# Kernel tuning notes

Measured on AMD Instinct MI355X. Metric: run time of the kernel, lower is better.

## Reference

```python
import jax, jax.numpy as jnp
import numpy as np

B, T, N, H, L, K, E, KSEL = 16, 24, 2000, 64, 2, 2, 3, 2
OUT_LEN = 24
NUM_MAT = 1 + 2 * K  # identity + K powers of each of the 2 supports


def _rw(adj):
    # random-walk matrix D^{-1} A
    d = adj.sum(axis=1)
    return adj / jnp.where(d == 0, 1.0, d)[:, None]


def _dconv(xh, A_q, A_h, W, b):
    # k-hop dual-direction diffusion convolution; xh: [b,n,f]
    feats = [xh]
    for A in (A_q, A_h):
        cur = xh
        for _ in range(K):
            cur = jnp.einsum('nm,bmf->bnf', A, cur)
            feats.append(cur)
    return jnp.concatenate(feats, axis=-1) @ W + b


def _cell(x, h, A_q, A_h, Wg, bg, Wc, bc):
    # DCRNN (diffusion-conv GRU) cell
    xh = jnp.concatenate([x, h], axis=-1)
    ru = jax.nn.sigmoid(_dconv(xh, A_q, A_h, Wg, bg))
    r, u = jnp.split(ru, 2, axis=-1)
    c = jnp.tanh(_dconv(jnp.concatenate([x, r * h], axis=-1), A_q, A_h, Wc, bc))
    return u * h + (1.0 - u) * c


def setup_inputs() -> dict:
    key = jax.random.key(0)
    ks = jax.random.split(key, 24)
    s = 0.02
    nrm = lambda k, shp: (jax.random.normal(k, shp) * s).astype(jnp.float32)
    adj = (jax.random.uniform(ks[0], (N, N)) * (jax.random.uniform(ks[1], (N, N)) < 0.05)).astype(jnp.float32)
    x_enc = jax.random.normal(ks[2], (B, T, N, 1), dtype=jnp.float32)
    x_enc = x_enc * (jax.random.uniform(ks[3], (B, T, N, 1)) < 0.7)
    x_dec = jax.random.normal(ks[4], (B, OUT_LEN, N, 1), dtype=jnp.float32)

    def cell_p(k, fin):
        k1, k2 = jax.random.split(k)
        fcat = NUM_MAT * (fin + H)
        return (nrm(k1, (fcat, 2 * H)), jnp.zeros(2 * H, jnp.float32),
                nrm(k2, (fcat, H)), jnp.zeros(H, jnp.float32))

    e0 = cell_p(ks[5], 1)
    e1 = cell_p(ks[6], H)
    d0 = cell_p(ks[7], 1)
    d1 = cell_p(ks[8], H)
    return dict(
        adj=adj, x_enc=x_enc, x_dec=x_dec,
        gate_w1=nrm(ks[9], (T, H)), gate_b1=jnp.zeros(H, jnp.float32),
        gate_w2=nrm(ks[10], (H, E)), gate_b2=jnp.zeros(E, jnp.float32),
        ew_mean=nrm(ks[11], (T, T)), eb_mean=jnp.zeros(T, jnp.float32),
        ew_wmean=nrm(ks[12], (T, T)), eb_wmean=jnp.zeros(T, jnp.float32),
        ew_diff=nrm(ks[13], (T, T)), eb_diff=jnp.zeros(T, jnp.float32),
        enc0_Wg=e0[0], enc0_bg=e0[1], enc0_Wc=e0[2], enc0_bc=e0[3],
        enc1_Wg=e1[0], enc1_bg=e1[1], enc1_Wc=e1[2], enc1_bc=e1[3],
        dec0_Wg=d0[0], dec0_bg=d0[1], dec0_Wc=d0[2], dec0_bc=d0[3],
        dec1_Wg=d1[0], dec1_bg=d1[1], dec1_Wc=d1[2], dec1_bc=d1[3],
        fc_w=nrm(ks[14], (H, 1)), fc_b=jnp.zeros(1, jnp.float32),
        epoch=10,
    )


def reference(adj, x_enc, x_dec, gate_w1, gate_b1, gate_w2, gate_b2,
              ew_mean, eb_mean, ew_wmean, eb_wmean, ew_diff, eb_diff,
              enc0_Wg, enc0_bg, enc0_Wc, enc0_bc, enc1_Wg, enc1_bg, enc1_Wc, enc1_bc,
              dec0_Wg, dec0_bg, dec0_Wc, dec0_bc, dec1_Wg, dec1_bg, dec1_Wc, dec1_bc,
              fc_w, fc_b, epoch):
    A_q = _rw(adj)
    A_h = _rw(adj.T)

    # ---- DataPreparation: MoE-gated graph imputation ----
    x = jnp.transpose(x_enc[..., 0], (0, 2, 1))  # [b, n, t]
    g = jax.nn.relu(x @ gate_w1 + gate_b1)
    logits = g @ gate_w2 + gate_b2               # [b, n, E]
    top, idx = jax.lax.top_k(logits, KSEL)
    w = jax.nn.softmax(top, axis=-1)
    gate = (w[..., None] * jax.nn.one_hot(idx, E, dtype=x.dtype)).sum(axis=-2)  # [b,n,E]

    adj_ns = adj * (1.0 - jnp.eye(N, dtype=adj.dtype))
    deg_bin = (adj_ns > 0).astype(x.dtype)
    A_mean = deg_bin / jnp.maximum(deg_bin.sum(axis=1, keepdims=True), 1.0)
    rs = adj_ns.sum(axis=1, keepdims=True)
    A_wmean = adj_ns / jnp.where(rs == 0, 1.0, rs)
    A_diff = _rw(adj_ns)

    outs = [jnp.einsum('nm,bmt->bnt', A_agg, x) @ W + b
            for A_agg, W, b in ((A_mean, ew_mean, eb_mean),
                                (A_wmean, ew_wmean, eb_wmean),
                                (A_diff, ew_diff, eb_diff))]
    combined = (gate[..., None] * jnp.stack(outs, axis=2)).sum(axis=2)  # [b,n,t]
    x = jnp.where(x == 0, combined, x)
    x_imp = jnp.transpose(x, (0, 2, 1))[..., None]  # [b,t,n,1]

    # ---- Encoder: scan over time, 2 DCRNN layers ----
    enc_params = ((enc0_Wg, enc0_bg, enc0_Wc, enc0_bc),
                  (enc1_Wg, enc1_bg, enc1_Wc, enc1_bc))

    def enc_step(h, xt):
        inp = xt
        hs = []
        for l in range(L):
            nh = _cell(inp, h[l], A_q, A_h, *enc_params[l])
            inp = nh
            hs.append(nh)
        return jnp.stack(hs), None

    h0 = jnp.zeros((L, B, N, H), x_imp.dtype)
    hT, _ = jax.lax.scan(enc_step, h0, jnp.transpose(x_imp, (1, 0, 2, 3)))

    dec_params = ((dec0_Wg, dec0_bg, dec0_Wc, dec0_bc),
                  (dec1_Wg, dec1_bg, dec1_Wc, dec1_bc))

    def dec_step(carry, _):
        inp, h = carry
        hs = []
        for l in range(L):
            nh = _cell(inp, h[l], A_q, A_h, *dec_params[l])
            inp = nh
            hs.append(nh)
        out = nh @ fc_w + fc_b  # [b,n,1]
        return (out, jnp.stack(hs)), out

    _, outs_t = jax.lax.scan(dec_step, (x_imp[:, -1], hT), None, length=OUT_LEN)
    return jnp.transpose(outs_t, (1, 0, 2, 3))  # [b, out_len, n, 1]
```

## Files before the change

kernel.cpp:

```cpp
#include <hip/hip_runtime.h>

#define NROW 2000
#define NB   16
#define NT   24
#define NH   64
#define NM   (NROW*NB)
#define HOPLDS (NROW*80)
#define ENT_CAP 262144

typedef _Float16 h16;
typedef __attribute__((ext_vector_type(2))) _Float16 h16x2;
typedef __attribute__((ext_vector_type(8))) _Float16 h16x8;
typedef __attribute__((ext_vector_type(4))) float    f32x4;

__device__ __forceinline__ h16x2 bc_h2(unsigned int u){ union{unsigned int u; h16x2 h;} c; c.u=u; return c.h; }

__global__ __launch_bounds__(256) void k_count(const float* adj, int* cnt_q, int* cnt_h, int* cnt_ns,
    float* rsum_q, float* rsum_h, float* rsum_ns, int* deg_ns){
  int wid = (blockIdx.x*256 + threadIdx.x)>>6;
  int lane = threadIdx.x & 63;
  int kind = wid / NROW, n = wid - kind*NROW;
  int cnt = 0; float sum = 0.f;
  for (int c = lane; c < NROW; c += 64){
    float v = (kind==1) ? adj[(size_t)c*NROW + n] : adj[(size_t)n*NROW + c];
    if (kind==2 && c==n) v = 0.f;
    cnt += (v != 0.f); sum += v;
  }
  for (int off=32; off; off>>=1){ cnt += __shfl_down(cnt,off); sum += __shfl_down(sum,off); }
  if (lane==0){
    int pc = (cnt+7)&~7;
    if (kind==0){ cnt_q[n]=pc; rsum_q[n]=sum; }
    else if (kind==1){ cnt_h[n]=pc; rsum_h[n]=sum; }
    else { cnt_ns[n]=pc; rsum_ns[n]=sum; deg_ns[n]=cnt; }
  }
}

__global__ __launch_bounds__(1024) void k_scan(const int* cq, const int* ch, const int* cn,
    int* rq, int* rh, int* rn){
  __shared__ int s0[2048], s1[2048], s2[2048];
  int t = threadIdx.x;
  for (int a=0;a<2;a++){ int i=t+a*1024; s0[i]= i<NROW?cq[i]:0; s1[i]= i<NROW?ch[i]:0; s2[i]= i<NROW?cn[i]:0; }
  __syncthreads();
  for (int off=1; off<2048; off<<=1){
    int v0[2],v1[2],v2[2];
    for (int a=0;a<2;a++){ int i=t+a*1024; v0[a]= i>=off? s0[i-off]:0; v1[a]= i>=off? s1[i-off]:0; v2[a]= i>=off? s2[i-off]:0; }
    __syncthreads();
    for (int a=0;a<2;a++){ int i=t+a*1024; s0[i]+=v0[a]; s1[i]+=v1[a]; s2[i]+=v2[a]; }
    __syncthreads();
  }
  for (int a=0;a<2;a++){ int i=t+a*1024; if (i<=NROW){ rq[i]= i? s0[i-1]:0; rh[i]= i? s1[i-1]:0; rn[i]= i? s2[i-1]:0; } }
}

__device__ __forceinline__ uint2 mk_ent(int c, float a){
  h16 h = (h16)a;
  unsigned short us = __builtin_bit_cast(unsigned short, h);
  return make_uint2((unsigned int)(c*80), (unsigned int)us * 0x10001u);
}

__global__ __launch_bounds__(256) void k_fill(const float* adj, const int* rptr_q, const int* rptr_h, const int* rptr_ns,
    const float* rsum_q, const float* rsum_h, const float* rsum_ns, const int* deg_ns,
    uint2* ent_q, uint2* ent_h, uint2* ent_m, uint2* ent_w){
  int wid = (blockIdx.x*256 + threadIdx.x)>>6;
  int lane = threadIdx.x & 63;
  int kind = wid / NROW, n = wid - kind*NROW;
  const int* rp = (kind==0)?rptr_q:(kind==1)?rptr_h:rptr_ns;
  int p = rp[n], pend = rp[n+1];
  float inv, invm = 0.f;
  if (kind==0){ float d = rsum_q[n]; inv = d!=0.f?1.f/d:0.f; }
  else if (kind==1){ float d = rsum_h[n]; inv = d!=0.f?1.f/d:0.f; }
  else { float d = rsum_ns[n]; inv = d!=0.f?1.f/d:0.f; int dg = deg_ns[n]; invm = 1.f/(float)(dg>1?dg:1); }
  int base = 0;
  unsigned long long below = (1ull<<lane)-1ull;
  for (int c0=0; c0<NROW; c0+=64){
    int c = c0+lane; float v = 0.f;
    if (c < NROW){ v = (kind==1)? adj[(size_t)c*NROW+n] : adj[(size_t)n*NROW+c]; if (kind==2 && c==n) v = 0.f; }
    unsigned long long m = __ballot(v != 0.f);
    if (v != 0.f){
      int pos = p + base + __popcll(m & below);
      if (kind==2){ ent_w[pos] = mk_ent(c, v*inv); ent_m[pos] = mk_ent(c, invm); }
      else if (kind==0) ent_q[pos] = mk_ent(c, v*inv);
      else              ent_h[pos] = mk_ent(c, v*inv);
    }
    base += __popcll(m);
  }
  for (int i = p+base+lane; i < pend; i += 64){
    uint2 z = make_uint2(0u,0u);
    if (kind==2){ ent_w[i]=z; ent_m[i]=z; } else if (kind==0) ent_q[i]=z; else ent_h[i]=z;
  }
}

struct HopJob { const h16* X; const int* rptr; const uint2* ent; h16* out; };

__device__ __forceinline__ void proc2(const char* xs, int cl, uint4 p, h16x2 ha[4]){
  union{f32x4 v; h16x2 h[4];} ca, cb;
  ca.v = *(const f32x4*)(xs + p.x + cl);
  cb.v = *(const f32x4*)(xs + p.z + cl);
  h16x2 va = bc_h2(p.y), vb = bc_h2(p.w);
  ha[0] = ca.h[0]*va + ha[0];
  ha[1] = ca.h[1]*va + ha[1];
  ha[2] = ca.h[2]*va + ha[2];
  ha[3] = ca.h[3]*va + ha[3];
  ha[0] = cb.h[0]*vb + ha[0];
  ha[1] = cb.h[1]*vb + ha[1];
  ha[2] = cb.h[2]*vb + ha[2];
  ha[3] = cb.h[3]*vb + ha[3];
}

__global__ __launch_bounds__(1024) void k_hop(HopJob j0, HopJob j1, HopJob j2, HopJob j3,
                                              int coltiles, int rsplit, int rows_per, int C){
  extern __shared__ char xs[];
  int per = coltiles*rsplit;
  int bid = blockIdx.x;
  int jb = bid/per, rem = bid - jb*per;
  int ct = rem/rsplit, rs = rem - ct*rsplit;
  HopJob j = (jb==0)?j0:(jb==1)?j1:(jb==2)?j2:j3;
  int c0 = ct*32;
  int tid = threadIdx.x;
  {
    int r0 = tid>>2, so = tid&3;
    const char* src = (const char*)j.X + (size_t)2*(c0 + so*8);
    char* dst = xs + so*16;
    for (int r = r0; r < NROW; r += 256)
      *(f32x4*)(dst + r*80) = *(const f32x4*)(src + (size_t)2*r*C);
  }
  __syncthreads();
  int lane = tid&63, wv = tid>>6;
  int g = lane>>2;
  int cl = (lane&3)*16;
  int rbase = rs*rows_per;
  int rend = rbase + rows_per; if (rend > NROW) rend = NROW;
  int units = (rows_per+15)>>4;
  for (int u = wv; u < units; u += 16){
    int n = rbase + u*16 + g;
    if (n < rend){
      int p0 = j.rptr[n], cnt = j.rptr[n+1]-p0;
      const uint4* ep4 = (const uint4*)(j.ent + p0);
      float f[8] = {0.f,0.f,0.f,0.f,0.f,0.f,0.f,0.f};
      if (cnt > 0){
        uint4 e0 = ep4[0], e1 = ep4[1], e2 = ep4[2], e3 = ep4[3];
        for (int i=0; i<cnt; i+=8){
          uint4 n0,n1,n2,n3;
          if (i+8 < cnt){
            int b = (i>>1)+4;
            n0 = ep4[b]; n1 = ep4[b+1]; n2 = ep4[b+2]; n3 = ep4[b+3];
          }
          h16x2 ha[4] = {{(_Float16)0.f,(_Float16)0.f},{(_Float16)0.f,(_Float16)0.f},
                         {(_Float16)0.f,(_Float16)0.f},{(_Float16)0.f,(_Float16)0.f}};
          proc2(xs, cl, e0, ha);
          proc2(xs, cl, e1, ha);
          proc2(xs, cl, e2, ha);
          proc2(xs, cl, e3, ha);
          f[0] += (float)ha[0][0]; f[1] += (float)ha[0][1];
          f[2] += (float)ha[1][0]; f[3] += (float)ha[1][1];
          f[4] += (float)ha[2][0]; f[5] += (float)ha[2][1];
          f[6] += (float)ha[3][0]; f[7] += (float)ha[3][1];
          e0=n0; e1=n1; e2=n2; e3=n3;
        }
      }
      alignas(16) h16 ov[8];
      #pragma unroll
      for (int k2=0;k2<8;k2++) ov[k2] = (h16)f[k2];
      *(uint4*)((char*)j.out + (size_t)2*((size_t)n*C + c0) + cl) = *(const uint4*)ov;
    }
  }
}

__global__ void k_evinit(const float* rq, const float* rh, float* eq, float* eh){
  int n = blockIdx.x*256+threadIdx.x; if (n>=NROW) return;
  eq[n] = rq[n]!=0.f?1.f:0.f; eh[n] = rh[n]!=0.f?1.f:0.f;
}

__global__ __launch_bounds__(256) void k_matvec(const int* rptr, const uint2* ent, const float* vin, float* vout){
  int wid = (blockIdx.x*256+threadIdx.x)>>6; int lane = threadIdx.x&63;
  if (wid >= NROW) return;
  int p0 = rptr[wid], p1 = rptr[wid+1];
  float s = 0.f;
  for (int i=p0+lane; i<p1; i+=64){
    uint2 e = ent[i];
    int idx = (int)(e.x/80u);
    h16 hv = __builtin_bit_cast(h16, (unsigned short)(e.y & 0xffffu));
    s += (float)hv * vin[idx];
  }
  for (int off=32; off; off>>=1) s += __shfl_down(s,off);
  if (lane==0) vout[wid] = s;
}

__global__ void k_bias2(const float* W, const float* fcb, const float* e1, const float* e2,
                        const float* e3, const float* e4, float* dst, int O){
  int idx = blockIdx.x*256+threadIdx.x; if (idx >= NROW*O) return;
  int n = idx/O, o = idx - n*O;
  float v = W[o] + e1[n]*W[(size_t)65*O+o] + e2[n]*W[(size_t)130*O+o]
                 + e3[n]*W[(size_t)195*O+o] + e4[n]*W[(size_t)260*O+o];
  dst[idx] = fcb[0]*v;
}

__global__ void k_wpack(const float* W, const float* fcw, h16* dst, int O, int nch, int mode){
  int idx = blockIdx.x*256+threadIdx.x; if (idx >= nch*O*32) return;
  int k = idx&31; int o = (idx>>5)%O; int ch = idx/(O*32);
  float v = 0.f;
  if (mode==0){
    if (ch < 10){ int m = ch>>1, j = (ch&1)*32 + k; v = W[(size_t)(m*65+1+j)*O + o]; }
    else if (k < 5) v = W[(size_t)(k*65)*O + o];
  } else if (mode==1){
    int m = ch>>2, j = (ch&3)*32 + k; v = W[(size_t)(m*128+j)*O + o];
  } else {
    if (ch < 10){ int m = ch>>1, j = (ch&1)*32 + k; v = fcw[j]*W[(size_t)(m*65)*O + o]; }
    else { int c2 = ch-10; int m = c2>>1, j = (c2&1)*32 + k; v = W[(size_t)(m*65+1+j)*O + o]; }
  }
  dst[(size_t)(ch*O + o)*32 + k] = (h16)v;
}

__global__ __launch_bounds__(256) void k_impute_gate(const float* x_enc, const float* gw1, const float* gb1,
    const float* gw2, const float* gb2, float* gate3, h16* xT){
  int tid = blockIdx.x*256+threadIdx.x; if (tid >= NM) return;
  int b = tid / NROW, n = tid - b*NROW;
  float x24[NT];
  #pragma unroll
  for (int t=0;t<NT;t++) x24[t] = x_enc[((size_t)b*NT+t)*NROW + n];
  float acc[NH];
  #pragma unroll
  for (int h=0;h<NH;h++) acc[h] = gb1[h];
  for (int t=0;t<NT;t++){
    float xv = x24[t];
    #pragma unroll
    for (int h=0;h<NH;h++) acc[h] = fmaf(xv, gw1[t*NH+h], acc[h]);
  }
  #pragma unroll
  for (int h=0;h<NH;h++) acc[h] = fmaxf(acc[h], 0.f);
  float lg[3];
  #pragma unroll
  for (int e=0;e<3;e++){
    float s = gb2[e];
    #pragma unroll
    for (int h=0;h<NH;h++) s = fmaf(acc[h], gw2[h*3+e], s);
    lg[e] = s;
  }
  int i0 = 0; if (lg[1] > lg[0]) i0 = 1; if (lg[2] > lg[i0]) i0 = 2;
  int i1 = (i0==0)?1:0;
  for (int e=0;e<3;e++) if (e!=i0 && e!=i1 && lg[e] > lg[i1]) i1 = e;
  float w1 = expf(lg[i1]-lg[i0]);
  float s = 1.f + w1;
  float g[3] = {0.f,0.f,0.f};
  g[i0] = 1.f/s; g[i1] = w1/s;
  gate3[tid*3+0]=g[0]; gate3[tid*3+1]=g[1]; gate3[tid*3+2]=g[2];
  h16* xp = xT + ((size_t)n*NB + b)*NT;
  #pragma unroll
  for (int t=0;t<NT;t++) xp[t] = (h16)x24[t];
}

__global__ __launch_bounds__(256) void k_impute_combine(const float* x_enc, const h16* Zm, const h16* Zw,
    const float* gate3, const float* ewm, const float* ebm, const float* eww, const float* ebw,
    const float* ewd, const float* ebd, h16* ximp){
  int tid = blockIdx.x*256+threadIdx.x; if (tid >= NM) return;
  int b = tid / NROW, n = tid - b*NROW;
  float x24[NT], zm[NT], zw[NT];
  const h16* zp1 = Zm + ((size_t)n*NB+b)*NT;
  const h16* zp2 = Zw + ((size_t)n*NB+b)*NT;
  #pragma unroll
  for (int t=0;t<NT;t++){ x24[t] = x_enc[((size_t)b*NT+t)*NROW + n]; zm[t]=(float)zp1[t]; zw[t]=(float)zp2[t]; }
  float g0=gate3[tid*3], g1=gate3[tid*3+1], g2=gate3[tid*3+2];
  h16* op = ximp + ((size_t)n*NB+b)*NT;
  for (int t=0;t<NT;t++){
    float am=ebm[t], aw=ebw[t], ad=ebd[t];
    #pragma unroll
    for (int ss=0;ss<NT;ss++){ am = fmaf(zm[ss], ewm[ss*NT+t], am); aw = fmaf(zw[ss], eww[ss*NT+t], aw); ad = fmaf(zw[ss], ewd[ss*NT+t], ad); }
    float comb = g0*am + g1*aw + g2*ad;
    op[t] = (h16)((x24[t]==0.f)? comb : x24[t]);
  }
}

__global__ void k_xpack8(const h16* ximp, const h16* xq1, const h16* xq2, const h16* xh1, const h16* xh2, h16* xp){
  int idx = blockIdx.x*256+threadIdx.x; if (idx >= NT*NM) return;
  int t = idx/NM, r = idx - t*NM;
  size_t s = (size_t)r*NT + t;
  alignas(16) h16 v[8] = { ximp[s], xq1[s], xq2[s], xh1[s], xh2[s], (h16)0.f,(h16)0.f,(h16)0.f };
  *(uint4*)(xp + ((size_t)t*NM + r)*8) = *(const uint4*)v;
}

struct GArgs {
  const h16* src[20];
  int rstrideB[20];
  int coffB[20];
  const h16* wpack;
  const float* bias;
  const h16* hbuf;
  h16* rhbuf;
  float* ubuf;
  h16* hout;
  const float* bias2;
  const float* fcw;
  const float* fcb;
  float* dout;
  int tstep;
  int nchunks;
  int xchunk;
};

template<int O, int GATE, int BIAS2, int FCOUT>
__global__ __launch_bounds__(256) void k_g(GArgs a){
  __shared__ h16 As[128*40];
  __shared__ h16 Bs[O*40];
  const int tid = threadIdx.x;
  const int lane = tid&63, wv = tid>>6;
  const int l15 = lane&15, l4 = lane>>4;
  const int mbase = blockIdx.x*128;
  f32x4 acc[2][O/16];
  #pragma unroll
  for (int rf=0;rf<2;rf++)
    #pragma unroll
    for (int cf=0;cf<O/16;cf++) acc[rf][cf] = (f32x4){0.f,0.f,0.f,0.f};

  f32x4 ra[2], rb[2];
  const f32x4 vz = (f32x4){0.f,0.f,0.f,0.f};
  auto loadA = [&](int ch){
    const char* sp = (const char*)a.src[ch] + a.coffB[ch] + (size_t)mbase*a.rstrideB[ch];
    if (ch == a.xchunk){
      int r = tid>>1;
      ra[1] = vz;
      ra[0] = (tid&1) ? vz : *(const f32x4*)(sp + (size_t)r*16);
    } else {
      int rs = a.rstrideB[ch];
      #pragma unroll
      for (int ps=0; ps<2; ps++){
        int flat = ps*256+tid; int r = flat>>2, q = flat&3;
        ra[ps] = *(const f32x4*)(sp + (size_t)r*rs + q*16);
      }
    }
    const char* wp = (const char*)a.wpack + (size_t)ch*O*64;
    #pragma unroll
    for (int ps=0; ps<O/64; ps++){
      int flat = ps*256+tid;
      rb[ps] = *(const f32x4*)(wp + (size_t)flat*16);
    }
  };
  auto writeA = [&](int ch){
    if (ch == a.xchunk){
      int r = tid>>1; int half = (tid&1)*32;
      *(f32x4*)((char*)As + r*80 + half)      = ra[0];
      *(f32x4*)((char*)As + r*80 + half + 16) = ra[1];
    } else {
      #pragma unroll
      for (int ps=0; ps<2; ps++){
        int flat = ps*256+tid; int r = flat>>2, q = flat&3;
        *(f32x4*)((char*)As + r*80 + q*16) = ra[ps];
      }
    }
    #pragma unroll
    for (int ps=0; ps<O/64; ps++){
      int flat = ps*256+tid; int r = flat>>2, q = flat&3;
      *(f32x4*)((char*)Bs + r*80 + q*16) = rb[ps];
    }
  };

  loadA(0);
  for (int ch=0; ch<a.nchunks; ch++){
    writeA(ch);
    __syncthreads();
    if (ch+1 < a.nchunks) loadA(ch+1);
    h16x8 a0 = *(const h16x8*)((const char*)As + (wv*32 + l15)*80 + l4*16);
    h16x8 a1 = *(const h16x8*)((const char*)As + (wv*32 + 16 + l15)*80 + l4*16);
    #pragma unroll
    for (int cf=0; cf<O/16; cf++){
      h16x8 bfr = *(const h16x8*)((const char*)Bs + (cf*16 + l15)*80 + l4*16);
      acc[0][cf] = __builtin_amdgcn_mfma_f32_16x16x32_f16(a0, bfr, acc[0][cf], 0,0,0);
      acc[1][cf] = __builtin_amdgcn_mfma_f32_16x16x32_f16(a1, bfr, acc[1][cf], 0,0,0);
    }
    __syncthreads();
  }
  float fcp[8] = {0.f,0.f,0.f,0.f,0.f,0.f,0.f,0.f};
  #pragma unroll
  for (int rf=0; rf<2; rf++){
    #pragma unroll
    for (int cf=0; cf<O/16; cf++){
      #pragma unroll
      for (int i=0;i<4;i++){
        int row = mbase + wv*32 + rf*16 + l4*4 + i;
        int col = cf*16 + l15;
        float v = acc[rf][cf][i] + a.bias[col];
        if (BIAS2) v += a.bias2[(size_t)(row>>4)*O + col];
        if (GATE){
          float sg = 1.f/(1.f+expf(-v));
          if (cf*16 < NH){
            float hv = (float)a.hbuf[(size_t)row*NH + col];
            a.rhbuf[(size_t)row*NH + col] = (h16)(sg*hv);
          } else {
            a.ubuf[(size_t)row*NH + (col-NH)] = sg;
          }
        } else {
          float cc = tanhf(v);
          float u  = a.ubuf[(size_t)row*NH + col];
          float hv = (float)a.hbuf[(size_t)row*NH + col];
          float hn = u*hv + (1.f-u)*cc;
          a.hout[(size_t)row*NH + col] = (h16)hn;
          if (FCOUT) fcp[rf*4+i] += hn * a.fcw[col];
        }
      }
    }
  }
  if (FCOUT){
    #pragma unroll
    for (int k=0;k<8;k++){
      float s = fcp[k];
      s += __shfl_xor(s,1); s += __shfl_xor(s,2); s += __shfl_xor(s,4); s += __shfl_xor(s,8);
      if (l15==0){
        int rf = k>>2, i = k&3;
        int row = mbase + wv*32 + rf*16 + l4*4 + i;
        int n = row>>4, b = row&15;
        a.dout[(size_t)b*(NT*NROW) + (size_t)a.tstep*NROW + n] = s + a.fcb[0];
      }
    }
  }
}

extern "C" void kernel_launch(void* const* d_in, const int* in_sizes, int n_in,
                              void* d_out, int out_size, void* d_ws, size_t ws_size,
                              hipStream_t stream)
{
  const float* adj   = (const float*)d_in[0];
  const float* x_enc = (const float*)d_in[1];
  const float* gw1   = (const float*)d_in[3];
  const float* gb1   = (const float*)d_in[4];
  const float* gw2   = (const float*)d_in[5];
  const float* gb2   = (const float*)d_in[6];
  const float* ewm   = (const float*)d_in[7];
  const float* ebm   = (const float*)d_in[8];
  const float* eww   = (const float*)d_in[9];
  const float* ebw   = (const float*)d_in[10];
  const float* ewd   = (const float*)d_in[11];
  const float* ebd   = (const float*)d_in[12];
  const float* Wg[4] = {(const float*)d_in[13],(const float*)d_in[17],(const float*)d_in[21],(const float*)d_in[25]};
  const float* bg[4] = {(const float*)d_in[14],(const float*)d_in[18],(const float*)d_in[22],(const float*)d_in[26]};
  const float* Wc[4] = {(const float*)d_in[15],(const float*)d_in[19],(const float*)d_in[23],(const float*)d_in[27]};
  const float* bc[4] = {(const float*)d_in[16],(const float*)d_in[20],(const float*)d_in[24],(const float*)d_in[28]};
  const float* fcw   = (const float*)d_in[29];
  const float* fcb   = (const float*)d_in[30];
  float* outp = (float*)d_out;
  (void)in_sizes; (void)n_in; (void)out_size; (void)ws_size;

  char* base = (char*)d_ws;
  size_t off = 0;
  auto alloc = [&](size_t sz)->char*{ char* p = base + off; off += (sz + 255) & ~(size_t)255; return p; };

  uint2* ent_q = (uint2*)alloc(ENT_CAP*8);
  uint2* ent_h = (uint2*)alloc(ENT_CAP*8);
  uint2* ent_m = (uint2*)alloc(ENT_CAP*8);
  uint2* ent_w = (uint2*)alloc(ENT_CAP*8);
  int* rptr_q = (int*)alloc(2001*4);
  int* rptr_h = (int*)alloc(2001*4);
  int* rptr_n = (int*)alloc(2001*4);
  int* cnt_q = (int*)alloc(NROW*4);
  int* cnt_h = (int*)alloc(NROW*4);
  int* cnt_n = (int*)alloc(NROW*4);
  float* rsum_q = (float*)alloc(NROW*4);
  float* rsum_h = (float*)alloc(NROW*4);
  float* rsum_n = (float*)alloc(NROW*4);
  int* deg_n = (int*)alloc(NROW*4);
  float* evq1 = (float*)alloc(NROW*4);
  float* evq2 = (float*)alloc(NROW*4);
  float* evh1 = (float*)alloc(NROW*4);
  float* evh2 = (float*)alloc(NROW*4);
  float* gate3 = (float*)alloc((size_t)NM*3*4);
  h16* xpack = (h16*)alloc((size_t)NT*NM*8*2);
  h16* wp_e0g = (h16*)alloc(11*128*64); h16* wp_e0c = (h16*)alloc(11*64*64);
  h16* wp_e1g = (h16*)alloc(20*128*64); h16* wp_e1c = (h16*)alloc(20*64*64);
  h16* wp_d0gE= (h16*)alloc(11*128*64); h16* wp_d0cE= (h16*)alloc(11*64*64);
  h16* wp_d0gW= (h16*)alloc(20*128*64); h16* wp_d0cW= (h16*)alloc(20*64*64);
  h16* wp_d1g = (h16*)alloc(20*128*64); h16* wp_d1c = (h16*)alloc(20*64*64);
  float* bias2g = (float*)alloc((size_t)NROW*128*4);
  float* bias2c = (float*)alloc((size_t)NROW*64*4);
  const size_t SEG = (size_t)NM*NH*2;
  h16* h0 = (h16*)alloc(SEG);
  h16* h1 = (h16*)alloc(SEG);
  float* ub = (float*)alloc((size_t)NM*NH*4);
  h16* rh = (h16*)alloc(SEG);
  h16* zb = (h16*)alloc(SEG);
  h16* H0Q1=(h16*)alloc(SEG); h16* H0Q2=(h16*)alloc(SEG); h16* H0H1=(h16*)alloc(SEG); h16* H0H2=(h16*)alloc(SEG);
  h16* H1Q1=(h16*)alloc(SEG); h16* H1Q2=(h16*)alloc(SEG); h16* H1H1=(h16*)alloc(SEG); h16* H1H2=(h16*)alloc(SEG);
  h16* RHQ1=(h16*)alloc(SEG); h16* RHQ2=(h16*)alloc(SEG); h16* RHH1=(h16*)alloc(SEG); h16* RHH2=(h16*)alloc(SEG);
  h16* xT   = RHQ1;  h16* Zm = RHQ2;  h16* Zw = RHH1;  h16* ximp = RHH2;
  h16* xq1  = H1Q1;  h16* xq2 = H1Q2; h16* xh1 = H1H1; h16* xh2 = H1H2;

  hipFuncSetAttribute(reinterpret_cast<const void*>(k_hop),
                      hipFuncAttributeMaxDynamicSharedMemorySize, HOPLDS);

  hipMemsetAsync(zb, 0, SEG, stream);
  hipMemsetAsync(h0, 0, SEG, stream);
  hipMemsetAsync(h1, 0, SEG, stream);

  k_count<<<1500,256,0,stream>>>(adj, cnt_q, cnt_h, cnt_n, rsum_q, rsum_h, rsum_n, deg_n);
  k_scan<<<1,1024,0,stream>>>(cnt_q, cnt_h, cnt_n, rptr_q, rptr_h, rptr_n);
  k_fill<<<1500,256,0,stream>>>(adj, rptr_q, rptr_h, rptr_n, rsum_q, rsum_h, rsum_n, deg_n,
                                ent_q, ent_h, ent_m, ent_w);
  k_evinit<<<8,256,0,stream>>>(rsum_q, rsum_h, evq1, evh1);
  k_matvec<<<500,256,0,stream>>>(rptr_q, ent_q, evq1, evq2);
  k_matvec<<<500,256,0,stream>>>(rptr_h, ent_h, evh1, evh2);
  k_bias2<<<1000,256,0,stream>>>(Wg[2], fcb, evq1, evq2, evh1, evh2, bias2g, 128);
  k_bias2<<<500,256,0,stream>>>(Wc[2], fcb, evq1, evq2, evh1, evh2, bias2c, 64);
  auto wpk = [&](const float* W, h16* dst, int O, int nch, int mode){
    k_wpack<<<(nch*O*32+255)/256,256,0,stream>>>(W, fcw, dst, O, nch, mode);
  };
  wpk(Wg[0], wp_e0g, 128, 11, 0); wpk(Wc[0], wp_e0c, 64, 11, 0);
  wpk(Wg[1], wp_e1g, 128, 20, 1); wpk(Wc[1], wp_e1c, 64, 20, 1);
  wpk(Wg[2], wp_d0gE,128, 11, 0); wpk(Wc[2], wp_d0cE,64, 11, 0);
  wpk(Wg[2], wp_d0gW,128, 20, 2); wpk(Wc[2], wp_d0cW,64, 20, 2);
  wpk(Wg[3], wp_d1g, 128, 20, 1); wpk(Wc[3], wp_d1c, 64, 20, 1);

  k_impute_gate<<<125,256,0,stream>>>(x_enc, gw1, gb1, gw2, gb2, gate3, xT);

  auto hop = [&](HopJob a, HopJob b, HopJob c, HopJob d, int nj, int C, int rsplit){
    int ct = C/32;
    k_hop<<<nj*ct*rsplit, 1024, HOPLDS, stream>>>(a,b,c,d, ct, rsplit, NROW/rsplit, C);
  };
  HopJob JA{xT, rptr_n, ent_m, Zm}, JB{xT, rptr_n, ent_w, Zw};
  hop(JA, JB, JA, JB, 2, NB*NT, 10);
  k_impute_combine<<<125,256,0,stream>>>(x_enc, Zm, Zw, gate3, ewm, ebm, eww, ebw, ewd, ebd, ximp);
  HopJob X1{ximp, rptr_q, ent_q, xq1}, X2{ximp, rptr_h, ent_h, xh1};
  hop(X1, X2, X1, X2, 2, NB*NT, 10);
  HopJob X3{xq1, rptr_q, ent_q, xq2}, X4{xh1, rptr_h, ent_h, xh2};
  hop(X3, X4, X3, X4, 2, NB*NT, 10);
  k_xpack8<<<(NT*NM+255)/256,256,0,stream>>>(ximp, xq1, xq2, xh1, xh2, xpack);

  h16* HSEG0[5] = {h0, H0Q1, H0Q2, H0H1, H0H2};
  h16* HSEG1[5] = {h1, H1Q1, H1Q2, H1H1, H1H2};
  h16* RSEG[5]  = {rh, RHQ1, RHQ2, RHH1, RHH2};
  h16* ZSEG[5]  = {zb, zb, zb, zb, zb};

  auto shapeA = [&](GArgs& A, h16* const* seg, const h16* xpk){
    for (int m=0;m<5;m++) for (int s=0;s<2;s++){ int ch=2*m+s; A.src[ch]=seg[m]; A.rstrideB[ch]=NH*2; A.coffB[ch]=s*64; }
    A.src[10]=xpk; A.rstrideB[10]=16; A.coffB[10]=0; A.nchunks=11; A.xchunk=10;
  };
  auto shapeB = [&](GArgs& A, h16* const* sa, h16* const* sb){
    for (int m=0;m<5;m++) for (int s=0;s<4;s++){ int ch=4*m+s;
      A.src[ch] = (s<2)? sa[m] : sb[m]; A.rstrideB[ch]=NH*2; A.coffB[ch]=(s&1)*64; }
    A.nchunks=20; A.xchunk=-1;
  };
  auto shapeC = [&](GArgs& A, h16* const* segH, h16* const* segX){
    for (int m=0;m<5;m++) for (int s=0;s<2;s++){
      int ch=2*m+s; A.src[ch]=segX[m]; A.rstrideB[ch]=NH*2; A.coffB[ch]=s*64;
      int c2=10+2*m+s; A.src[c2]=segH[m]; A.rstrideB[c2]=NH*2; A.coffB[c2]=s*64; }
    A.nchunks=20; A.xchunk=-1;
  };
  auto common = [&](GArgs& A, const h16* wp, const float* bias, const h16* hb, const float* b2, int t){
    A.wpack=wp; A.bias=bias; A.hbuf=hb; A.rhbuf=rh; A.ubuf=ub; A.hout=(h16*)hb;
    A.bias2=b2; A.fcw=fcw; A.fcb=fcb; A.dout=outp; A.tstep=t;
  };

  for (int phase=0; phase<2; phase++){
    int ig = phase? 2 : 0;
    const h16* wpg0E = phase? wp_d0gE : wp_e0g;
    const h16* wpc0E = phase? wp_d0cE : wp_e0c;
    const h16* wpg1  = phase? wp_d1g  : wp_e1g;
    const h16* wpc1  = phase? wp_d1c  : wp_e1c;
    for (int t=0;t<NT;t++){
      bool wprime = (phase==1 && t>0);
      if (wprime){
        HopJob a{h1, rptr_q, ent_q, H1Q1}, b{h1, rptr_h, ent_h, H1H1};
        hop(a,b,a,b, 2, NB*NH, 4);
        HopJob c{H1Q1, rptr_q, ent_q, H1Q2}, d{H1H1, rptr_h, ent_h, H1H2};
        hop(c,d,c,d, 2, NB*NH, 4);
      }
      {
        GArgs A{};
        if (wprime) shapeC(A, HSEG0, HSEG1);
        else shapeA(A, (phase==0 && t==0)? ZSEG : HSEG0, xpack + (size_t)((phase==0)? t : 23)*NM*8);
        common(A, wprime? wp_d0gW : wpg0E, bg[ig], h0, bias2g, t);
        if (wprime) k_g<128,1,1,0><<<250,256,0,stream>>>(A);
        else        k_g<128,1,0,0><<<250,256,0,stream>>>(A);
      }
      if (wprime){
        HopJob a{rh, rptr_q, ent_q, RHQ1}, b{rh, rptr_h, ent_h, RHH1};
        hop(a,b,a,b, 2, NB*NH, 4);
        HopJob c{RHQ1, rptr_q, ent_q, RHQ2}, d{RHH1, rptr_h, ent_h, RHH2};
        hop(c,d,c,d, 2, NB*NH, 4);
      } else {
        HopJob a{rh, rptr_q, ent_q, RHQ1}, b{rh, rptr_h, ent_h, RHH1};
        HopJob c{h1, rptr_q, ent_q, H1Q1}, d{h1, rptr_h, ent_h, H1H1};
        hop(a,b,c,d, 4, NB*NH, 2);
        HopJob a2{RHQ1, rptr_q, ent_q, RHQ2}, b2{RHH1, rptr_h, ent_h, RHH2};
        HopJob c2{H1Q1, rptr_q, ent_q, H1Q2}, d2{H1H1, rptr_h, ent_h, H1H2};
        hop(a2,b2,c2,d2, 4, NB*NH, 2);
      }
      {
        GArgs A{};
        if (wprime) shapeC(A, RSEG, HSEG1);
        else shapeA(A, RSEG, xpack + (size_t)((phase==0)? t : 23)*NM*8);
        common(A, wprime? wp_d0cW : wpc0E, bc[ig], h0, bias2c, t);
        if (wprime) k_g<64,0,1,0><<<250,256,0,stream>>>(A);
        else        k_g<64,0,0,0><<<250,256,0,stream>>>(A);
      }
      {
        HopJob a{h0, rptr_q, ent_q, H0Q1}, b{h0, rptr_h, ent_h, H0H1};
        hop(a,b,a,b, 2, NB*NH, 4);
        HopJob c{H0Q1, rptr_q, ent_q, H0Q2}, d{H0H1, rptr_h, ent_h, H0H2};
        hop(c,d,c,d, 2, NB*NH, 4);
      }
      {
        GArgs A{};
        shapeB(A, HSEG0, HSEG1);
        common(A, wpg1, bg[ig+1], h1, nullptr, t);
        k_g<128,1,0,0><<<250,256,0,stream>>>(A);
      }
      {
        HopJob a{rh, rptr_q, ent_q, RHQ1}, b{rh, rptr_h, ent_h, RHH1};
        hop(a,b,a,b, 2, NB*NH, 4);
        HopJob c{RHQ1, rptr_q, ent_q, RHQ2}, d{RHH1, rptr_h, ent_h, RHH2};
        hop(c,d,c,d, 2, NB*NH, 4);
      }
      {
        GArgs A{};
        shapeB(A, HSEG0, RSEG);
        common(A, wpc1, bc[ig+1], h1, nullptr, t);
        if (phase) k_g<64,0,0,1><<<250,256,0,stream>>>(A);
        else       k_g<64,0,0,0><<<250,256,0,stream>>>(A);
      }
    }
  }
}
```

Baseline: 16.19 ms.

## Halve GEMM row tile, unroll hop gather loop, unpad hop LDS rows

Three changes. The GEMM kernel's M tile drops from 128 to 64 rows per block, with one MFMA fragment per wave and 500 blocks instead of 250, to spread work over more CUs and lower register pressure. The sparse hop kernel now processes 16 entries per iteration with 8-deep prefetch and a tail of up to 8 entries. Its LDS row stride drops from 80 to 64 bytes, so index decoding becomes a shift instead of a divide, at the risk of LDS bank conflicts. Deeper prefetch raises register use in the hop kernel, and the smaller GEMM tile gives less reuse of weight tiles per block.

Result: faster. 13.50 ms (-16.6%).

```diff
diff --git a/kernel.cpp b/kernel.cpp
--- a/kernel.cpp
+++ b/kernel.cpp
@@ -5,7 +5,7 @@
 #define NT   24
 #define NH   64
 #define NM   (NROW*NB)
-#define HOPLDS (NROW*80)
+#define HOPLDS (NROW*64)
 #define ENT_CAP 262144
 
 typedef _Float16 h16;
@@ -54,7 +54,7 @@
 __device__ __forceinline__ uint2 mk_ent(int c, float a){
   h16 h = (h16)a;
   unsigned short us = __builtin_bit_cast(unsigned short, h);
-  return make_uint2((unsigned int)(c*80), (unsigned int)us * 0x10001u);
+  return make_uint2((unsigned int)(c*64), (unsigned int)us * 0x10001u);
 }
 
 __global__ __launch_bounds__(256) void k_fill(const float* adj, const int* rptr_q, const int* rptr_h, const int* rptr_ns,
@@ -121,7 +121,7 @@
     const char* src = (const char*)j.X + (size_t)2*(c0 + so*8);
     char* dst = xs + so*16;
     for (int r = r0; r < NROW; r += 256)
-      *(f32x4*)(dst + r*80) = *(const f32x4*)(src + (size_t)2*r*C);
+      *(f32x4*)(dst + r*64) = *(const f32x4*)(src + (size_t)2*r*C);
   }
   __syncthreads();
   int lane = tid&63, wv = tid>>6;
@@ -137,24 +137,37 @@
       const uint4* ep4 = (const uint4*)(j.ent + p0);
       float f[8] = {0.f,0.f,0.f,0.f,0.f,0.f,0.f,0.f};
       if (cnt > 0){
-        uint4 e0 = ep4[0], e1 = ep4[1], e2 = ep4[2], e3 = ep4[3];
-        for (int i=0; i<cnt; i+=8){
-          uint4 n0,n1,n2,n3;
-          if (i+8 < cnt){
-            int b = (i>>1)+4;
-            n0 = ep4[b]; n1 = ep4[b+1]; n2 = ep4[b+2]; n3 = ep4[b+3];
-          }
+        uint4 cur[8];
+        #pragma unroll
+        for (int u2=0;u2<8;u2++) cur[u2] = ep4[u2];
+        int i = 0;
+        for (; i+16 <= cnt; i += 16){
+          uint4 nx[8];
+          int b = (i>>1)+8;
+          #pragma unroll
+          for (int u2=0;u2<8;u2++) nx[u2] = ep4[b+u2];
           h16x2 ha[4] = {{(_Float16)0.f,(_Float16)0.f},{(_Float16)0.f,(_Float16)0.f},
                          {(_Float16)0.f,(_Float16)0.f},{(_Float16)0.f,(_Float16)0.f}};
-          proc2(xs, cl, e0, ha);
-          proc2(xs, cl, e1, ha);
-          proc2(xs, cl, e2, ha);
-          proc2(xs, cl, e3, ha);
+          #pragma unroll
+          for (int u2=0;u2<8;u2++) proc2(xs, cl, cur[u2], ha);
           f[0] += (float)ha[0][0]; f[1] += (float)ha[0][1];
           f[2] += (float)ha[1][0]; f[3] += (float)ha[1][1];
           f[4] += (float)ha[2][0]; f[5] += (float)ha[2][1];
           f[6] += (float)ha[3][0]; f[7] += (float)ha[3][1];
-          e0=n0; e1=n1; e2=n2; e3=n3;
+          #pragma unroll
+          for (int u2=0;u2<8;u2++) cur[u2] = nx[u2];
+        }
+        if (i < cnt){
+          h16x2 ha[4] = {{(_Float16)0.f,(_Float16)0.f},{(_Float16)0.f,(_Float16)0.f},
+                         {(_Float16)0.f,(_Float16)0.f},{(_Float16)0.f,(_Float16)0.f}};
+          proc2(xs, cl, cur[0], ha);
+          proc2(xs, cl, cur[1], ha);
+          proc2(xs, cl, cur[2], ha);
+          proc2(xs, cl, cur[3], ha);
+          f[0] += (float)ha[0][0]; f[1] += (float)ha[0][1];
+          f[2] += (float)ha[1][0]; f[3] += (float)ha[1][1];
+          f[4] += (float)ha[2][0]; f[5] += (float)ha[2][1];
+          f[6] += (float)ha[3][0]; f[7] += (float)ha[3][1];
         }
       }
       alignas(16) h16 ov[8];
@@ -177,7 +190,7 @@
   float s = 0.f;
   for (int i=p0+lane; i<p1; i+=64){
     uint2 e = ent[i];
-    int idx = (int)(e.x/80u);
+    int idx = (int)(e.x>>6);
     h16 hv = __builtin_bit_cast(h16, (unsigned short)(e.y & 0xffffu));
     s += (float)hv * vin[idx];
   }
@@ -298,33 +311,26 @@
 
 template<int O, int GATE, int BIAS2, int FCOUT>
 __global__ __launch_bounds__(256) void k_g(GArgs a){
-  __shared__ h16 As[128*40];
+  __shared__ h16 As[64*40];
   __shared__ h16 Bs[O*40];
   const int tid = threadIdx.x;
   const int lane = tid&63, wv = tid>>6;
   const int l15 = lane&15, l4 = lane>>4;
-  const int mbase = blockIdx.x*128;
-  f32x4 acc[2][O/16];
-  #pragma unroll
-  for (int rf=0;rf<2;rf++)
-    #pragma unroll
-    for (int cf=0;cf<O/16;cf++) acc[rf][cf] = (f32x4){0.f,0.f,0.f,0.f};
-
-  f32x4 ra[2], rb[2];
+  const int mbase = blockIdx.x*64;
+  f32x4 acc[O/16];
+  #pragma unroll
+  for (int cf=0;cf<O/16;cf++) acc[cf] = (f32x4){0.f,0.f,0.f,0.f};
+
+  f32x4 ra, rb[O/64 > 0 ? O/64 : 1];
   const f32x4 vz = (f32x4){0.f,0.f,0.f,0.f};
+  const int r_ = tid>>2, q_ = tid&3;
   auto loadA = [&](int ch){
     const char* sp = (const char*)a.src[ch] + a.coffB[ch] + (size_t)mbase*a.rstrideB[ch];
     if (ch == a.xchunk){
-      int r = tid>>1;
-      ra[1] = vz;
-      ra[0] = (tid&1) ? vz : *(const f32x4*)(sp + (size_t)r*16);
+      ra = q_ ? vz : *(const f32x4*)(sp + (size_t)r_*16);
     } else {
       int rs = a.rstrideB[ch];
-      #pragma unroll
-      for (int ps=0; ps<2; ps++){
-        int flat = ps*256+tid; int r = flat>>2, q = flat&3;
-        ra[ps] = *(const f32x4*)(sp + (size_t)r*rs + q*16);
-      }
+      ra = *(const f32x4*)(sp + (size_t)r_*rs + q_*16);
     }
     const char* wp = (const char*)a.wpack + (size_t)ch*O*64;
     #pragma unroll
@@ -334,17 +340,7 @@
     }
   };
   auto writeA = [&](int ch){
-    if (ch == a.xchunk){
-      int r = tid>>1; int half = (tid&1)*32;
-      *(f32x4*)((char*)As + r*80 + half)      = ra[0];
-      *(f32x4*)((char*)As + r*80 + half + 16) = ra[1];
-    } else {
-      #pragma unroll
-      for (int ps=0; ps<2; ps++){
-        int flat = ps*256+tid; int r = flat>>2, q = flat&3;
-        *(f32x4*)((char*)As + r*80 + q*16) = ra[ps];
-      }
-    }
+    *(f32x4*)((char*)As + r_*80 + q_*16) = ra;
     #pragma unroll
     for (int ps=0; ps<O/64; ps++){
       int flat = ps*256+tid; int r = flat>>2, q = flat&3;
@@ -357,54 +353,48 @@
     writeA(ch);
     __syncthreads();
     if (ch+1 < a.nchunks) loadA(ch+1);
-    h16x8 a0 = *(const h16x8*)((const char*)As + (wv*32 + l15)*80 + l4*16);
-    h16x8 a1 = *(const h16x8*)((const char*)As + (wv*32 + 16 + l15)*80 + l4*16);
+    h16x8 a0 = *(const h16x8*)((const char*)As + (wv*16 + l15)*80 + l4*16);
     #pragma unroll
     for (int cf=0; cf<O/16; cf++){
       h16x8 bfr = *(const h16x8*)((const char*)Bs + (cf*16 + l15)*80 + l4*16);
-      acc[0][cf] = __builtin_amdgcn_mfma_f32_16x16x32_f16(a0, bfr, acc[0][cf], 0,0,0);
-      acc[1][cf] = __builtin_amdgcn_mfma_f32_16x16x32_f16(a1, bfr, acc[1][cf], 0,0,0);
+      acc[cf] = __builtin_amdgcn_mfma_f32_16x16x32_f16(a0, bfr, acc[cf], 0,0,0);
     }
     __syncthreads();
   }
-  float fcp[8] = {0.f,0.f,0.f,0.f,0.f,0.f,0.f,0.f};
-  #pragma unroll
-  for (int rf=0; rf<2; rf++){
-    #pragma unroll
-    for (int cf=0; cf<O/16; cf++){
-      #pragma unroll
-      for (int i=0;i<4;i++){
-        int row = mbase + wv*32 + rf*16 + l4*4 + i;
-        int col = cf*16 + l15;
-        float v = acc[rf][cf][i] + a.bias[col];
-        if (BIAS2) v += a.bias2[(size_t)(row>>4)*O + col];
-        if (GATE){
-          float sg = 1.f/(1.f+expf(-v));
-          if (cf*16 < NH){
-            float hv = (float)a.hbuf[(size_t)row*NH + col];
-            a.rhbuf[(size_t)row*NH + col] = (h16)(sg*hv);
-          } else {
-            a.ubuf[(size_t)row*NH + (col-NH)] = sg;
-          }
+  float fcp[4] = {0.f,0.f,0.f,0.f};
+  #pragma unroll
+  for (int cf=0; cf<O/16; cf++){
+    #pragma unroll
+    for (int i=0;i<4;i++){
+      int row = mbase + wv*16 + l4*4 + i;
+      int col = cf*16 + l15;
+      float v = acc[cf][i] + a.bias[col];
+      if (BIAS2) v += a.bias2[(size_t)(row>>4)*O + col];
+      if (GATE){
+        float sg = 1.f/(1.f+expf(-v));
+        if (cf*16 < NH){
+          float hv = (float)a.hbuf[(size_t)row*NH + col];
+          a.rhbuf[(size_t)row*NH + col] = (h16)(sg*hv);
         } else {
-          float cc = tanhf(v);
-          float u  = a.ubuf[(size_t)row*NH + col];
-          float hv = (float)a.hbuf[(size_t)row*NH + col];
-          float hn = u*hv + (1.f-u)*cc;
-          a.hout[(size_t)row*NH + col] = (h16)hn;
-          if (FCOUT) fcp[rf*4+i] += hn * a.fcw[col];
+          a.ubuf[(size_t)row*NH + (col-NH)] = sg;
         }
+      } else {
+        float cc = tanhf(v);
+        float u  = a.ubuf[(size_t)row*NH + col];
+        float hv = (float)a.hbuf[(size_t)row*NH + col];
+        float hn = u*hv + (1.f-u)*cc;
+        a.hout[(size_t)row*NH + col] = (h16)hn;
+        if (FCOUT) fcp[i] += hn * a.fcw[col];
       }
     }
   }
   if (FCOUT){
     #pragma unroll
-    for (int k=0;k<8;k++){
+    for (int k=0;k<4;k++){
       float s = fcp[k];
       s += __shfl_xor(s,1); s += __shfl_xor(s,2); s += __shfl_xor(s,4); s += __shfl_xor(s,8);
       if (l15==0){
-        int rf = k>>2, i = k&3;
-        int row = mbase + wv*32 + rf*16 + l4*4 + i;
+        int row = mbase + wv*16 + l4*4 + k;
         int n = row>>4, b = row&15;
         a.dout[(size_t)b*(NT*NROW) + (size_t)a.tstep*NROW + n] = s + a.fcb[0];
       }
@@ -564,8 +554,8 @@
         if (wprime) shapeC(A, HSEG0, HSEG1);
         else shapeA(A, (phase==0 && t==0)? ZSEG : HSEG0, xpack + (size_t)((phase==0)? t : 23)*NM*8);
         common(A, wprime? wp_d0gW : wpg0E, bg[ig], h0, bias2g, t);
-        if (wprime) k_g<128,1,1,0><<<250,256,0,stream>>>(A);
-        else        k_g<128,1,0,0><<<250,256,0,stream>>>(A);
+        if (wprime) k_g<128,1,1,0><<<500,256,0,stream>>>(A);
+        else        k_g<128,1,0,0><<<500,256,0,stream>>>(A);
       }
       if (wprime){
         HopJob a{rh, rptr_q, ent_q, RHQ1}, b{rh, rptr_h, ent_h, RHH1};
@@ -585,8 +575,8 @@
         if (wprime) shapeC(A, RSEG, HSEG1);
         else shapeA(A, RSEG, xpack + (size_t)((phase==0)? t : 23)*NM*8);
         common(A, wprime? wp_d0cW : wpc0E, bc[ig], h0, bias2c, t);
-        if (wprime) k_g<64,0,1,0><<<250,256,0,stream>>>(A);
-        else        k_g<64,0,0,0><<<250,256,0,stream>>>(A);
+        if (wprime) k_g<64,0,1,0><<<500,256,0,stream>>>(A);
+        else        k_g<64,0,0,0><<<500,256,0,stream>>>(A);
       }
       {
         HopJob a{h0, rptr_q, ent_q, H0Q1}, b{h0, rptr_h, ent_h, H0H1};
@@ -598,7 +588,7 @@
         GArgs A{};
         shapeB(A, HSEG0, HSEG1);
         common(A, wpg1, bg[ig+1], h1, nullptr, t);
-        k_g<128,1,0,0><<<250,256,0,stream>>>(A);
+        k_g<128,1,0,0><<<500,256,0,stream>>>(A);
       }
       {
         HopJob a{rh, rptr_q, ent_q, RHQ1}, b{rh, rptr_h, ent_h, RHH1};
@@ -610,9 +600,9 @@
         GArgs A{};
         shapeB(A, HSEG0, RSEG);
         common(A, wpc1, bc[ig+1], h1, nullptr, t);
-        if (phase) k_g<64,0,0,1><<<250,256,0,stream>>>(A);
-        else       k_g<64,0,0,0><<<250,256,0,stream>>>(A);
-      }
-    }
-  }
-}
+        if (phase) k_g<64,0,0,1><<<500,256,0,stream>>>(A);
+        else       k_g<64,0,0,0><<<500,256,0,stream>>>(A);
+      }
+    }
+  }
+}
```
